# Kernel optimization log

Hardware: AMD Instinct MI355X
Metric: run time of the kernel (lower is better)

The kernel has to match this reference:

```python
import jax, jax.numpy as jnp
import numpy as np

B, S, D_IN, H, D_K = 4, 2048, 512, 8, 64
EPS = 1e-5

def _layer_norm(x, gamma, beta):
    mu = jnp.mean(x, axis=-1, keepdims=True)
    var = jnp.var(x, axis=-1, keepdims=True)
    return (x - mu) * jax.lax.rsqrt(var + EPS) * gamma + beta

def setup_inputs() -> dict:
    key = jax.random.key(0)
    ks = jax.random.split(key, 8)
    d_model = H * D_K
    scale = 1.0 / np.sqrt(D_IN)
    inp = {
        "q": jax.random.normal(ks[0], (B, S, D_IN), jnp.float32),
        "k": jax.random.normal(ks[1], (B, S, D_IN), jnp.float32),
        "v": jax.random.normal(ks[2], (B, S, D_IN), jnp.float32),
        "mask": jnp.ones((B, 1, S, S), jnp.float32),
        "Wq": jax.random.normal(ks[3], (D_IN, d_model), jnp.float32) * scale,
        "bq": jnp.zeros((d_model,), jnp.float32),
        "Wk": jax.random.normal(ks[4], (D_IN, d_model), jnp.float32) * scale,
        "bk": jnp.zeros((d_model,), jnp.float32),
        "Wv": jax.random.normal(ks[5], (D_IN, d_model), jnp.float32) * scale,
        "bv": jnp.zeros((d_model,), jnp.float32),
        "Wo": jax.random.normal(ks[6], (d_model, D_IN), jnp.float32) * (1.0 / np.sqrt(d_model)),
        "bo": jnp.zeros((D_IN,), jnp.float32),
        "gamma": jnp.ones((D_IN,), jnp.float32),
        "beta": jnp.zeros((D_IN,), jnp.float32),
    }
    return inp

def reference(q, k, v, mask, Wq, bq, Wk, bk, Wv, bv, Wo, bo, gamma, beta):
    b, sq, _ = q.shape
    # QKV projections, split heads: [B,S,H*Dk] -> [B,H,S,Dk]
    qh = (q @ Wq + bq).reshape(b, sq, H, D_K).transpose(0, 2, 1, 3)
    kh = (k @ Wk + bk).reshape(b, -1, H, D_K).transpose(0, 2, 1, 3)
    vh = (v @ Wv + bv).reshape(b, -1, H, D_K).transpose(0, 2, 1, 3)
    # scores with multiplicative mask + threshold (non-standard, per source)
    scores = jnp.einsum('bhqd,bhkd->bhqk', qh, kh) / np.sqrt(D_K)
    scores = scores * mask  # mask broadcasts over heads (repeat in torch)
    scores = jnp.where(scores > 0, scores, jnp.float32(-10000.0))
    attn = jax.nn.softmax(scores, axis=-1)
    out = jnp.einsum('bhqk,bhkd->bhqd', attn, vh)
    out = out.transpose(0, 2, 1, 3).reshape(b, sq, H * D_K)
    out = out @ Wo + bo
    return _layer_norm(q + out, gamma, beta)
```

## Files before the change

kernel.cpp:

```cpp
#include <hip/hip_runtime.h>
#include <stdint.h>

typedef __attribute__((ext_vector_type(8))) short s16x8;
typedef __attribute__((ext_vector_type(4))) float f32x4;

__device__ __forceinline__ unsigned short f2bf(float f){
  union { float f; unsigned u; } v; v.f = f;
  return (unsigned short)((v.u + 0x7FFFu + ((v.u>>16)&1u))>>16);
}
__device__ __forceinline__ float bf2f(unsigned short u){
  union { unsigned u; float f; } c; c.u = ((unsigned)u)<<16; return c.f;
}
#if __has_builtin(__builtin_amdgcn_cvt_pk_bf16_f32)
__device__ __forceinline__ unsigned pkbf(float a, float b){
  typedef __attribute__((ext_vector_type(2))) __bf16 bf16x2;
  union { bf16x2 v; unsigned u; } c;
  c.v = __builtin_amdgcn_cvt_pk_bf16_f32(a, b);
  return c.u;
}
#else
__device__ __forceinline__ unsigned pkbf(float a, float b){
  return (unsigned)f2bf(a) | ((unsigned)f2bf(b)<<16);
}
#endif

__device__ __forceinline__ void g2l16(const void* g, void* l){
  auto* lp = reinterpret_cast<__attribute__((address_space(3))) unsigned int*>(
      reinterpret_cast<uintptr_t>(l));
  auto* gp = reinterpret_cast<const __attribute__((address_space(1))) unsigned int*>(
      reinterpret_cast<uintptr_t>(g));
  __builtin_amdgcn_global_load_lds(gp, lp, 16, 0, 0);
}

__global__ __launch_bounds__(256) void cvt_all(
    const float* __restrict__ mask, const float* __restrict__ q,
    const float* __restrict__ k,    const float* __restrict__ v,
    unsigned short* __restrict__ mo, unsigned short* __restrict__ qo,
    unsigned short* __restrict__ ko, unsigned short* __restrict__ vo)
{
  const int z = blockIdx.z;
  const float* src = (z==0)?mask:(z==1)?q:(z==2)?k:v;
  unsigned short* dst = (z==0)?mo:(z==1)?qo:(z==2)?ko:vo;
  const int n = (z==0) ? 4*2048*2048 : 8192*512;
  const int i8 = (blockIdx.x*256 + threadIdx.x)*8;
  if (i8 < n){
    const float4 a = *(const float4*)&src[i8];
    const float4 b = *(const float4*)&src[i8+4];
    uint4 o;
    o.x = pkbf(a.x,a.y); o.y = pkbf(a.z,a.w);
    o.z = pkbf(b.x,b.y); o.w = pkbf(b.z,b.w);
    *(uint4*)&dst[i8] = o;
  }
}

__global__ __launch_bounds__(256) void convert_wT(
    const float* __restrict__ W0, const float* __restrict__ W1,
    const float* __restrict__ W2, const float* __restrict__ W3,
    unsigned short* __restrict__ T0, unsigned short* __restrict__ T1,
    unsigned short* __restrict__ T2, unsigned short* __restrict__ T3)
{
  __shared__ float Ts[64][65];
  const int z = blockIdx.z;
  const float* W = (z==0)?W0:(z==1)?W1:(z==2)?W2:W3;
  unsigned short* Wt = (z==0)?T0:(z==1)?T1:(z==2)?T2:T3;
  const int t = threadIdx.x;
  const int k0 = blockIdx.x*64, n0 = blockIdx.y*64;
  {
    const int r = t>>4, c = (t&15)*4;
#pragma unroll
    for (int rr=0; rr<4; ++rr){
      const float4 w4 = *(const float4*)&W[(size_t)(k0 + r + rr*16)*512 + n0 + c];
      Ts[r+rr*16][c]   = w4.x; Ts[r+rr*16][c+1] = w4.y;
      Ts[r+rr*16][c+2] = w4.z; Ts[r+rr*16][c+3] = w4.w;
    }
  }
  __syncthreads();
  const int n = t>>2, kc = (t&3)*16;
  unsigned o[8];
#pragma unroll
  for (int i=0;i<16;i+=2) o[i>>1] = pkbf(Ts[kc+i][n], Ts[kc+i+1][n]);
  *(uint4*)&Wt[(size_t)(n0+n)*512 + k0 + kc]     = *(uint4*)&o[0];
  *(uint4*)&Wt[(size_t)(n0+n)*512 + k0 + kc + 8] = *(uint4*)&o[4];
}

template<int EPI>
__global__ __launch_bounds__(256) void gemm_m97(
    const unsigned short* __restrict__ A0, const unsigned short* __restrict__ A1,
    const unsigned short* __restrict__ A2,
    const unsigned short* __restrict__ W0, const unsigned short* __restrict__ W1,
    const unsigned short* __restrict__ W2,
    const float* __restrict__ b0, const float* __restrict__ b1, const float* __restrict__ b2,
    unsigned short* __restrict__ Oq, unsigned short* __restrict__ Ok,
    unsigned short* __restrict__ Ov, unsigned short* __restrict__ Oflat)
{
  __shared__ unsigned short As[128*64];
  __shared__ unsigned short Bs[128*64];
  const int t = threadIdx.x;
  const int lane = t & 63;
  const int w = t >> 6;
  const int l16 = lane & 15;
  const int quad = lane >> 4;
  const int wm = w & 1, wn = w >> 1;
  const int bm = blockIdx.x, bn = blockIdx.y;
  const int z = (EPI==0) ? (int)blockIdx.z : 0;
  const unsigned short* A  = (z==0)?A0:(z==1)?A1:A2;
  const unsigned short* Wt = (z==0)?W0:(z==1)?W1:W2;
  const float* bias        = (z==0)?b0:(z==1)?b1:b2;

  const int Lr = lane >> 3;
  const int gc = (lane & 7) ^ Lr;

  f32x4 acc[4][4];
#pragma unroll
  for(int i=0;i<4;i++)
#pragma unroll
    for(int j=0;j<4;j++) acc[i][j] = (f32x4){0.f,0.f,0.f,0.f};

  for (int kt=0; kt<8; ++kt){
    const int k0 = kt*64;
#pragma unroll
    for (int j=0;j<4;++j){
      const int rb = w*32 + j*8;
      g2l16(&A [(size_t)(bm*128 + rb + Lr)*512 + k0 + gc*8], &As[rb*64]);
      g2l16(&Wt[(size_t)(bn*128 + rb + Lr)*512 + k0 + gc*8], &Bs[rb*64]);
    }
    __syncthreads();
#pragma unroll
    for (int kk=0;kk<2;++kk){
      s16x8 af[4], bfr[4];
#pragma unroll
      for (int mt=0;mt<4;++mt){
        const int row = wm*64 + mt*16 + l16;
        af[mt] = *(const s16x8*)&As[row*64 + (((kk*4+quad) ^ (row&7))*8)];
      }
#pragma unroll
      for (int nt=0;nt<4;++nt){
        const int row = wn*64 + nt*16 + l16;
        bfr[nt] = *(const s16x8*)&Bs[row*64 + (((kk*4+quad) ^ (row&7))*8)];
      }
#pragma unroll
      for (int mt=0;mt<4;++mt)
#pragma unroll
        for (int nt=0;nt<4;++nt)
          acc[mt][nt] = __builtin_amdgcn_mfma_f32_16x16x32_bf16(af[mt], bfr[nt], acc[mt][nt], 0,0,0);
    }
    __syncthreads();
  }

#pragma unroll
  for (int mt=0;mt<4;++mt){
    const int gm = bm*128 + wm*64 + mt*16 + quad*4;
    const int b_ = gm>>11, s = gm & 2047;
#pragma unroll
    for (int nt=0;nt<4;++nt){
      const int gn = bn*128 + wn*64 + nt*16 + l16;
      const float bv = bias[gn];
      if (EPI==1){
#pragma unroll
        for (int r=0;r<4;++r)
          Oflat[(size_t)(gm+r)*512 + gn] = f2bf(acc[mt][nt][r] + bv);
      } else if (z==2){
        const int hh = gn>>6, dk = gn&63;
        uint2 uu;
        uu.x = pkbf(acc[mt][nt][0]+bv, acc[mt][nt][1]+bv);
        uu.y = pkbf(acc[mt][nt][2]+bv, acc[mt][nt][3]+bv);
        *(uint2*)&Ov[(((size_t)b_*8 + hh)*64 + dk)*2048 + s] = uu;
      } else {
        const int hh = gn>>6, dk = gn&63;
        unsigned short* Out = (z==0)?Oq:Ok;
        const float scl = (z==0)?0.125f:1.0f;
#pragma unroll
        for (int r=0;r<4;++r)
          Out[(((size_t)b_*8 + hh)*2048 + (s+r))*64 + dk] = f2bf((acc[mt][nt][r]+bv)*scl);
      }
    }
  }
}

__global__ __launch_bounds__(512,4) void attn_kernel(
    const unsigned short* __restrict__ Qp, const unsigned short* __restrict__ Kp,
    const unsigned short* __restrict__ Vt, const unsigned short* __restrict__ maskb,
    unsigned short* __restrict__ Ap)
{
  __shared__ unsigned short Ks[2][64*64];
  __shared__ unsigned short Vs[2][64*64];
  const int t = threadIdx.x;
  const int lane = t & 63;
  const int w = t >> 6;
  const int l16 = lane & 15;
  const int quad = lane >> 4;
  const int h = blockIdx.x, qt = blockIdx.y, b = blockIdx.z;
  const int q0 = qt*128;
  const unsigned short* Qb = Qp + (((size_t)b*8 + h)*2048 + q0)*64;
  const unsigned short* Kb = Kp + ((size_t)b*8 + h)*2048*64;
  const unsigned short* Vb = Vt + ((size_t)b*8 + h)*64*2048;
  const unsigned short* mb = maskb + (size_t)b*2048*2048;

  s16x8 qf[2];
#pragma unroll
  for (int kk=0;kk<2;++kk)
    qf[kk] = *(const s16x8*)&Qb[(size_t)(w*16 + l16)*64 + kk*32 + quad*8];

  const int Lr = lane >> 3;
  const int gc = (lane & 7) ^ Lr;
  const int srow = w*8 + Lr;

  g2l16(&Kb[(size_t)srow*64   + gc*8], &Ks[0][w*8*64]);
  g2l16(&Vb[(size_t)srow*2048 + gc*8], &Vs[0][w*8*64]);

  f32x4 o_acc[4];
#pragma unroll
  for(int nt=0;nt<4;++nt) o_acc[nt]=(f32x4){0.f,0.f,0.f,0.f};
  float l_run = 0.f;

  union U8 { unsigned u[4]; s16x8 v; };
  const int gq = q0 + w*16 + l16;

  for (int kt=0; kt<32; ++kt){
    const int cur = kt&1;
    const int kbase = kt*64;
    __syncthreads();

    uint2 mr[4];
    {
      const unsigned short* mrow = mb + (size_t)gq*2048 + kbase + quad*4;
#pragma unroll
      for (int nt=0;nt<4;++nt) mr[nt] = *(const uint2*)&mrow[nt*16];
    }
    if (kt<31){
      const int kb2 = (kt+1)*64;
      g2l16(&Kb[(size_t)(kb2+srow)*64 + gc*8],   &Ks[cur^1][w*8*64]);
      g2l16(&Vb[(size_t)srow*2048 + kb2 + gc*8], &Vs[cur^1][w*8*64]);
    }

    f32x4 sc[4];
#pragma unroll
    for(int nt=0;nt<4;++nt) sc[nt]=(f32x4){0.f,0.f,0.f,0.f};
#pragma unroll
    for (int nt=0;nt<4;++nt){
      const int row = nt*16 + l16;
      const int rx = row & 7;
      const s16x8 kf0 = *(const s16x8*)&Ks[cur][row*64 + ((quad ^ rx)*8)];
      const s16x8 kf1 = *(const s16x8*)&Ks[cur][row*64 + (((4+quad) ^ rx)*8)];
      sc[nt] = __builtin_amdgcn_mfma_f32_16x16x32_bf16(kf0, qf[0], sc[nt],0,0,0);
      sc[nt] = __builtin_amdgcn_mfma_f32_16x16x32_bf16(kf1, qf[1], sc[nt],0,0,0);
    }
    unsigned pk[8];
    float rs = 0.f;
#pragma unroll
    for (int nt=0;nt<4;++nt){
      const float m0 = bf2f((unsigned short)(mr[nt].x & 0xffffu));
      const float m1 = bf2f((unsigned short)(mr[nt].x >> 16));
      const float m2 = bf2f((unsigned short)(mr[nt].y & 0xffffu));
      const float m3 = bf2f((unsigned short)(mr[nt].y >> 16));
      float x0 = sc[nt][0]*m0, x1 = sc[nt][1]*m1, x2 = sc[nt][2]*m2, x3 = sc[nt][3]*m3;
      x0 = (x0>0.f)?x0:-10000.f; x1 = (x1>0.f)?x1:-10000.f;
      x2 = (x2>0.f)?x2:-10000.f; x3 = (x3>0.f)?x3:-10000.f;
      const float e0 = __expf(x0), e1 = __expf(x1), e2 = __expf(x2), e3 = __expf(x3);
      rs += (e0+e1)+(e2+e3);
      pk[nt*2]   = pkbf(e0, e1);
      pk[nt*2+1] = pkbf(e2, e3);
    }
    rs += __shfl_xor(rs, 16);
    rs += __shfl_xor(rs, 32);
    l_run += rs;
    U8 pu[2];
#pragma unroll
    for (int kk=0;kk<2;++kk)
#pragma unroll
      for (int c=0;c<4;++c){
        const int srcLane = (((quad&1)*2 + (c>>1))<<4) | l16;
        const int vA = __shfl((int)pk[kk*4 + (c&1)],     srcLane);
        const int vB = __shfl((int)pk[kk*4 + 2 + (c&1)], srcLane);
        pu[kk].u[c] = (quad < 2) ? (unsigned)vA : (unsigned)vB;
      }
#pragma unroll
    for (int nt=0;nt<4;++nt){
      const int row = nt*16 + l16;
      const int rx = row & 7;
      const s16x8 vf0 = *(const s16x8*)&Vs[cur][row*64 + ((quad ^ rx)*8)];
      const s16x8 vf1 = *(const s16x8*)&Vs[cur][row*64 + (((4+quad) ^ rx)*8)];
      o_acc[nt] = __builtin_amdgcn_mfma_f32_16x16x32_bf16(vf0, pu[0].v, o_acc[nt],0,0,0);
      o_acc[nt] = __builtin_amdgcn_mfma_f32_16x16x32_bf16(vf1, pu[1].v, o_acc[nt],0,0,0);
    }
  }
  {
    const float inv = 1.0f / l_run;
#pragma unroll
    for (int nt=0;nt<4;++nt){
      uint2 uu;
      uu.x = pkbf(o_acc[nt][0]*inv, o_acc[nt][1]*inv);
      uu.y = pkbf(o_acc[nt][2]*inv, o_acc[nt][3]*inv);
      *(uint2*)&Ap[((size_t)b*2048 + gq)*512 + h*64 + nt*16 + quad*4] = uu;
    }
  }
}

__global__ __launch_bounds__(256) void ln_kernel(
    const float* __restrict__ q, const unsigned short* __restrict__ O2,
    const float* __restrict__ gamma, const float* __restrict__ beta,
    float* __restrict__ out)
{
  const int r = blockIdx.x;
  const int t = threadIdx.x;
  const float* xq = q + (size_t)r * 512;
  const unsigned short* xo = O2 + (size_t)r * 512;
  const float x0 = xq[t]       + bf2f(xo[t]);
  const float x1 = xq[t + 256] + bf2f(xo[t + 256]);
  float s  = x0 + x1;
  float ss = x0*x0 + x1*x1;
#pragma unroll
  for (int off = 1; off < 64; off <<= 1) {
    s  += __shfl_xor(s, off);
    ss += __shfl_xor(ss, off);
  }
  __shared__ float ssum[4], ssq[4];
  const int w = t >> 6;
  if ((t & 63) == 0) { ssum[w] = s; ssq[w] = ss; }
  __syncthreads();
  const float S4 = ssum[0] + ssum[1] + ssum[2] + ssum[3];
  const float Q4 = ssq[0] + ssq[1] + ssq[2] + ssq[3];
  const float mu   = S4 * (1.0f / 512.0f);
  const float var  = Q4 * (1.0f / 512.0f) - mu * mu;
  const float rstd = rsqrtf(var + 1e-5f);
  out[(size_t)r*512 + t]       = (x0 - mu)*rstd*gamma[t] + beta[t];
  out[(size_t)r*512 + t + 256] = (x1 - mu)*rstd*gamma[t+256] + beta[t+256];
}

extern "C" void kernel_launch(void* const* d_in, const int* in_sizes, int n_in,
                              void* d_out, int out_size, void* d_ws, size_t ws_size,
                              hipStream_t stream)
{
  (void)in_sizes; (void)n_in; (void)out_size; (void)ws_size;
  const float* q    = (const float*)d_in[0];
  const float* k    = (const float*)d_in[1];
  const float* v    = (const float*)d_in[2];
  const float* mask = (const float*)d_in[3];
  const float* Wq   = (const float*)d_in[4];
  const float* bq   = (const float*)d_in[5];
  const float* Wk   = (const float*)d_in[6];
  const float* bk   = (const float*)d_in[7];
  const float* Wv   = (const float*)d_in[8];
  const float* bv   = (const float*)d_in[9];
  const float* Wo   = (const float*)d_in[10];
  const float* bo   = (const float*)d_in[11];
  const float* gamma = (const float*)d_in[12];
  const float* beta  = (const float*)d_in[13];
  float* out = (float*)d_out;

  const size_t NT = (size_t)8192*512;
  unsigned short* WtQ  = (unsigned short*)d_ws;
  unsigned short* WtK  = WtQ + 512*512;
  unsigned short* WtV  = WtK + 512*512;
  unsigned short* WtO  = WtV + 512*512;
  unsigned short* Mb   = WtO + 512*512;
  unsigned short* qb   = Mb + (size_t)4*2048*2048;
  unsigned short* kb   = qb + NT;
  unsigned short* vb   = kb + NT;
  unsigned short* Qp   = vb + NT;
  unsigned short* Kp   = Qp + NT;
  unsigned short* Vtg  = Kp + NT;
  unsigned short* Ap   = Vtg + NT;
  unsigned short* O2b  = Ap + NT;

  cvt_all<<<dim3(8192,1,4), 256, 0, stream>>>(mask, q, k, v, Mb, qb, kb, vb);
  convert_wT<<<dim3(8,8,4), 256, 0, stream>>>(Wq, Wk, Wv, Wo, WtQ, WtK, WtV, WtO);
  gemm_m97<0><<<dim3(64,4,3), 256, 0, stream>>>(qb, kb, vb, WtQ, WtK, WtV,
                                                bq, bk, bv, Qp, Kp, Vtg, nullptr);
  attn_kernel<<<dim3(8,16,4), 512, 0, stream>>>(Qp, Kp, Vtg, Mb, Ap);
  gemm_m97<1><<<dim3(64,4,1), 256, 0, stream>>>(Ap, nullptr, nullptr, WtO, nullptr, nullptr,
                                                bo, nullptr, nullptr,
                                                nullptr, nullptr, nullptr, O2b);
  ln_kernel<<<dim3(8192), 256, 0, stream>>>(q, O2b, gamma, beta, out);
}
```

Before: 311.3 us.

## Read fp32 mask directly in attention and give each wave two query tiles

Removes the separate fp32-to-bf16 pass over the full mask and its bf16 workspace copy, so the attention kernel now reads the fp32 mask itself. The attention block drops from 8 waves to 4, and each wave handles 32 query rows (two 16-row tiles), so every K/V fragment read from LDS feeds two MFMAs. K and V LDS tiles get a new fragment-ordered, padded layout. The trade-off is twice as many mask bytes read inside the attention loop per step, higher register pressure from the doubled accumulators, and fewer waves per block.

```diff
diff --git a/kernel.cpp b/kernel.cpp
--- a/kernel.cpp
+++ b/kernel.cpp
@@ -32,25 +32,20 @@
   __builtin_amdgcn_global_load_lds(gp, lp, 16, 0, 0);
 }
 
-__global__ __launch_bounds__(256) void cvt_all(
-    const float* __restrict__ mask, const float* __restrict__ q,
-    const float* __restrict__ k,    const float* __restrict__ v,
-    unsigned short* __restrict__ mo, unsigned short* __restrict__ qo,
-    unsigned short* __restrict__ ko, unsigned short* __restrict__ vo)
+__global__ __launch_bounds__(256) void cvt_qkv(
+    const float* __restrict__ q, const float* __restrict__ k, const float* __restrict__ v,
+    unsigned short* __restrict__ qo, unsigned short* __restrict__ ko, unsigned short* __restrict__ vo)
 {
   const int z = blockIdx.z;
-  const float* src = (z==0)?mask:(z==1)?q:(z==2)?k:v;
-  unsigned short* dst = (z==0)?mo:(z==1)?qo:(z==2)?ko:vo;
-  const int n = (z==0) ? 4*2048*2048 : 8192*512;
+  const float* src = (z==0)?q:(z==1)?k:v;
+  unsigned short* dst = (z==0)?qo:(z==1)?ko:vo;
   const int i8 = (blockIdx.x*256 + threadIdx.x)*8;
-  if (i8 < n){
-    const float4 a = *(const float4*)&src[i8];
-    const float4 b = *(const float4*)&src[i8+4];
-    uint4 o;
-    o.x = pkbf(a.x,a.y); o.y = pkbf(a.z,a.w);
-    o.z = pkbf(b.x,b.y); o.w = pkbf(b.z,b.w);
-    *(uint4*)&dst[i8] = o;
-  }
+  const float4 a = *(const float4*)&src[i8];
+  const float4 b = *(const float4*)&src[i8+4];
+  uint4 o;
+  o.x = pkbf(a.x,a.y); o.y = pkbf(a.z,a.w);
+  o.z = pkbf(b.x,b.y); o.w = pkbf(b.z,b.w);
+  *(uint4*)&dst[i8] = o;
 }
 
 __global__ __launch_bounds__(256) void convert_wT(
@@ -177,121 +172,141 @@
   }
 }
 
-__global__ __launch_bounds__(512,4) void attn_kernel(
+__global__ __launch_bounds__(256,2) void attn_kernel(
     const unsigned short* __restrict__ Qp, const unsigned short* __restrict__ Kp,
-    const unsigned short* __restrict__ Vt, const unsigned short* __restrict__ maskb,
+    const unsigned short* __restrict__ Vt, const float* __restrict__ mask,
     unsigned short* __restrict__ Ap)
 {
-  __shared__ unsigned short Ks[2][64*64];
-  __shared__ unsigned short Vs[2][64*64];
+  __shared__ unsigned short Ks[2][8*512];
+  __shared__ unsigned short Vs[2][8*528];
   const int t = threadIdx.x;
   const int lane = t & 63;
   const int w = t >> 6;
   const int l16 = lane & 15;
   const int quad = lane >> 4;
   const int h = blockIdx.x, qt = blockIdx.y, b = blockIdx.z;
-  const int q0 = qt*128;
-  const unsigned short* Qb = Qp + (((size_t)b*8 + h)*2048 + q0)*64;
+  const int q0 = qt*128 + w*32;
+  const unsigned short* Qb = Qp + ((size_t)b*8 + h)*2048*64;
   const unsigned short* Kb = Kp + ((size_t)b*8 + h)*2048*64;
   const unsigned short* Vb = Vt + ((size_t)b*8 + h)*64*2048;
-  const unsigned short* mb = maskb + (size_t)b*2048*2048;
-
-  s16x8 qf[2];
-#pragma unroll
-  for (int kk=0;kk<2;++kk)
-    qf[kk] = *(const s16x8*)&Qb[(size_t)(w*16 + l16)*64 + kk*32 + quad*8];
-
-  const int Lr = lane >> 3;
-  const int gc = (lane & 7) ^ Lr;
-  const int srow = w*8 + Lr;
-
-  g2l16(&Kb[(size_t)srow*64   + gc*8], &Ks[0][w*8*64]);
-  g2l16(&Vb[(size_t)srow*2048 + gc*8], &Vs[0][w*8*64]);
-
-  f32x4 o_acc[4];
-#pragma unroll
-  for(int nt=0;nt<4;++nt) o_acc[nt]=(f32x4){0.f,0.f,0.f,0.f};
-  float l_run = 0.f;
+  const float* mb = mask + (size_t)b*2048*2048;
+
+  s16x8 qf[2][2];
+#pragma unroll
+  for (int tc=0;tc<2;++tc)
+#pragma unroll
+    for (int kk=0;kk<2;++kk)
+      qf[tc][kk] = *(const s16x8*)&Qb[(size_t)(q0 + tc*16 + l16)*64 + kk*32 + quad*8];
+
+  int koffs[2], voffs[2];
+#pragma unroll
+  for (int j=0;j<2;++j){
+    koffs[j] = ((w*16 + (lane&15))*64) + ((j*4 + (lane>>4))*8);
+    voffs[j] = (((2*w+j)*8 + (lane>>3))*2048) + (((lane&7) ^ (lane>>3))*8);
+  }
+#pragma unroll
+  for (int j=0;j<2;++j){
+    g2l16(Kb + koffs[j], &Ks[0][(2*w+j)*512]);
+    g2l16(Vb + voffs[j], &Vs[0][(2*w+j)*528]);
+  }
+
+  f32x4 o_acc[2][4];
+#pragma unroll
+  for(int tc=0;tc<2;++tc)
+#pragma unroll
+    for(int nt=0;nt<4;++nt) o_acc[tc][nt]=(f32x4){0.f,0.f,0.f,0.f};
+  float l_run[2] = {0.f, 0.f};
+
+  const int b3 = l16>>3, a7 = l16&7;
+  const float* mrow0 = mb + (size_t)(q0 + l16)*2048 + quad*4;
+  const float* mrow1 = mrow0 + (size_t)16*2048;
 
   union U8 { unsigned u[4]; s16x8 v; };
-  const int gq = q0 + w*16 + l16;
 
   for (int kt=0; kt<32; ++kt){
     const int cur = kt&1;
     const int kbase = kt*64;
     __syncthreads();
 
-    uint2 mr[4];
-    {
-      const unsigned short* mrow = mb + (size_t)gq*2048 + kbase + quad*4;
-#pragma unroll
-      for (int nt=0;nt<4;++nt) mr[nt] = *(const uint2*)&mrow[nt*16];
+    float4 mr[2][4];
+#pragma unroll
+    for (int nt=0;nt<4;++nt){
+      mr[0][nt] = *(const float4*)&mrow0[kbase + nt*16];
+      mr[1][nt] = *(const float4*)&mrow1[kbase + nt*16];
     }
     if (kt<31){
       const int kb2 = (kt+1)*64;
-      g2l16(&Kb[(size_t)(kb2+srow)*64 + gc*8],   &Ks[cur^1][w*8*64]);
-      g2l16(&Vb[(size_t)srow*2048 + kb2 + gc*8], &Vs[cur^1][w*8*64]);
-    }
-
-    f32x4 sc[4];
-#pragma unroll
-    for(int nt=0;nt<4;++nt) sc[nt]=(f32x4){0.f,0.f,0.f,0.f};
-#pragma unroll
-    for (int nt=0;nt<4;++nt){
-      const int row = nt*16 + l16;
-      const int rx = row & 7;
-      const s16x8 kf0 = *(const s16x8*)&Ks[cur][row*64 + ((quad ^ rx)*8)];
-      const s16x8 kf1 = *(const s16x8*)&Ks[cur][row*64 + (((4+quad) ^ rx)*8)];
-      sc[nt] = __builtin_amdgcn_mfma_f32_16x16x32_bf16(kf0, qf[0], sc[nt],0,0,0);
-      sc[nt] = __builtin_amdgcn_mfma_f32_16x16x32_bf16(kf1, qf[1], sc[nt],0,0,0);
-    }
-    unsigned pk[8];
-    float rs = 0.f;
-#pragma unroll
-    for (int nt=0;nt<4;++nt){
-      const float m0 = bf2f((unsigned short)(mr[nt].x & 0xffffu));
-      const float m1 = bf2f((unsigned short)(mr[nt].x >> 16));
-      const float m2 = bf2f((unsigned short)(mr[nt].y & 0xffffu));
-      const float m3 = bf2f((unsigned short)(mr[nt].y >> 16));
-      float x0 = sc[nt][0]*m0, x1 = sc[nt][1]*m1, x2 = sc[nt][2]*m2, x3 = sc[nt][3]*m3;
-      x0 = (x0>0.f)?x0:-10000.f; x1 = (x1>0.f)?x1:-10000.f;
-      x2 = (x2>0.f)?x2:-10000.f; x3 = (x3>0.f)?x3:-10000.f;
-      const float e0 = __expf(x0), e1 = __expf(x1), e2 = __expf(x2), e3 = __expf(x3);
-      rs += (e0+e1)+(e2+e3);
-      pk[nt*2]   = pkbf(e0, e1);
-      pk[nt*2+1] = pkbf(e2, e3);
-    }
-    rs += __shfl_xor(rs, 16);
-    rs += __shfl_xor(rs, 32);
-    l_run += rs;
-    U8 pu[2];
-#pragma unroll
-    for (int kk=0;kk<2;++kk)
-#pragma unroll
-      for (int c=0;c<4;++c){
-        const int srcLane = (((quad&1)*2 + (c>>1))<<4) | l16;
-        const int vA = __shfl((int)pk[kk*4 + (c&1)],     srcLane);
-        const int vB = __shfl((int)pk[kk*4 + 2 + (c&1)], srcLane);
-        pu[kk].u[c] = (quad < 2) ? (unsigned)vA : (unsigned)vB;
-      }
-#pragma unroll
-    for (int nt=0;nt<4;++nt){
-      const int row = nt*16 + l16;
-      const int rx = row & 7;
-      const s16x8 vf0 = *(const s16x8*)&Vs[cur][row*64 + ((quad ^ rx)*8)];
-      const s16x8 vf1 = *(const s16x8*)&Vs[cur][row*64 + (((4+quad) ^ rx)*8)];
-      o_acc[nt] = __builtin_amdgcn_mfma_f32_16x16x32_bf16(vf0, pu[0].v, o_acc[nt],0,0,0);
-      o_acc[nt] = __builtin_amdgcn_mfma_f32_16x16x32_bf16(vf1, pu[1].v, o_acc[nt],0,0,0);
-    }
-  }
-  {
-    const float inv = 1.0f / l_run;
-#pragma unroll
-    for (int nt=0;nt<4;++nt){
+#pragma unroll
+      for (int j=0;j<2;++j){
+        g2l16(Kb + (size_t)kb2*64 + koffs[j], &Ks[cur^1][(2*w+j)*512]);
+        g2l16(Vb + kb2 + voffs[j],            &Vs[cur^1][(2*w+j)*528]);
+      }
+    }
+
+    f32x4 sc[2][4];
+#pragma unroll
+    for(int tc=0;tc<2;++tc)
+#pragma unroll
+      for(int nt=0;nt<4;++nt) sc[tc][nt]=(f32x4){0.f,0.f,0.f,0.f};
+#pragma unroll
+    for (int nt=0;nt<4;++nt)
+#pragma unroll
+      for (int kk=0;kk<2;++kk){
+        const s16x8 kf = *(const s16x8*)&Ks[cur][(nt*2+kk)*512 + lane*8];
+#pragma unroll
+        for (int tc=0;tc<2;++tc)
+          sc[tc][nt] = __builtin_amdgcn_mfma_f32_16x16x32_bf16(kf, qf[tc][kk], sc[tc][nt],0,0,0);
+      }
+
+#pragma unroll
+    for (int tc=0;tc<2;++tc){
+      unsigned pk[8];
+      float rs = 0.f;
+#pragma unroll
+      for (int nt=0;nt<4;++nt){
+        float x0 = sc[tc][nt][0]*mr[tc][nt].x, x1 = sc[tc][nt][1]*mr[tc][nt].y;
+        float x2 = sc[tc][nt][2]*mr[tc][nt].z, x3 = sc[tc][nt][3]*mr[tc][nt].w;
+        x0 = (x0>0.f)?x0:-10000.f; x1 = (x1>0.f)?x1:-10000.f;
+        x2 = (x2>0.f)?x2:-10000.f; x3 = (x3>0.f)?x3:-10000.f;
+        const float e0 = __expf(x0), e1 = __expf(x1), e2 = __expf(x2), e3 = __expf(x3);
+        rs += (e0+e1)+(e2+e3);
+        pk[nt*2]   = pkbf(e0, e1);
+        pk[nt*2+1] = pkbf(e2, e3);
+      }
+      rs += __shfl_xor(rs, 16);
+      rs += __shfl_xor(rs, 32);
+      l_run[tc] += rs;
+      U8 pu[2];
+#pragma unroll
+      for (int kk=0;kk<2;++kk)
+#pragma unroll
+        for (int c=0;c<4;++c){
+          const int srcLane = (((quad&1)*2 + (c>>1))<<4) | l16;
+          const int vA = __shfl((int)pk[kk*4 + (c&1)],     srcLane);
+          const int vB = __shfl((int)pk[kk*4 + 2 + (c&1)], srcLane);
+          pu[kk].u[c] = (quad < 2) ? (unsigned)vA : (unsigned)vB;
+        }
+#pragma unroll
+      for (int ot=0;ot<4;++ot){
+#pragma unroll
+        for (int kk=0;kk<2;++kk){
+          const s16x8 vf = *(const s16x8*)&Vs[cur][(ot*2+b3)*528 + a7*64 + (((kk*4+quad)^a7)*8)];
+          o_acc[tc][ot] = __builtin_amdgcn_mfma_f32_16x16x32_bf16(vf, pu[kk].v, o_acc[tc][ot],0,0,0);
+        }
+      }
+    }
+  }
+
+#pragma unroll
+  for (int tc=0;tc<2;++tc){
+    const float inv = 1.0f / l_run[tc];
+    const int gq = q0 + tc*16 + l16;
+#pragma unroll
+    for (int ot=0;ot<4;++ot){
       uint2 uu;
-      uu.x = pkbf(o_acc[nt][0]*inv, o_acc[nt][1]*inv);
-      uu.y = pkbf(o_acc[nt][2]*inv, o_acc[nt][3]*inv);
-      *(uint2*)&Ap[((size_t)b*2048 + gq)*512 + h*64 + nt*16 + quad*4] = uu;
+      uu.x = pkbf(o_acc[tc][ot][0]*inv, o_acc[tc][ot][1]*inv);
+      uu.y = pkbf(o_acc[tc][ot][2]*inv, o_acc[tc][ot][3]*inv);
+      *(uint2*)&Ap[((size_t)b*2048 + gq)*512 + h*64 + ot*16 + quad*4] = uu;
     }
   }
 }
@@ -353,8 +368,7 @@
   unsigned short* WtK  = WtQ + 512*512;
   unsigned short* WtV  = WtK + 512*512;
   unsigned short* WtO  = WtV + 512*512;
-  unsigned short* Mb   = WtO + 512*512;
-  unsigned short* qb   = Mb + (size_t)4*2048*2048;
+  unsigned short* qb   = WtO + 512*512;
   unsigned short* kb   = qb + NT;
   unsigned short* vb   = kb + NT;
   unsigned short* Qp   = vb + NT;
@@ -363,11 +377,11 @@
   unsigned short* Ap   = Vtg + NT;
   unsigned short* O2b  = Ap + NT;
 
-  cvt_all<<<dim3(8192,1,4), 256, 0, stream>>>(mask, q, k, v, Mb, qb, kb, vb);
+  cvt_qkv<<<dim3(2048,1,3), 256, 0, stream>>>(q, k, v, qb, kb, vb);
   convert_wT<<<dim3(8,8,4), 256, 0, stream>>>(Wq, Wk, Wv, Wo, WtQ, WtK, WtV, WtO);
   gemm_m97<0><<<dim3(64,4,3), 256, 0, stream>>>(qb, kb, vb, WtQ, WtK, WtV,
                                                 bq, bk, bv, Qp, Kp, Vtg, nullptr);
-  attn_kernel<<<dim3(8,16,4), 512, 0, stream>>>(Qp, Kp, Vtg, Mb, Ap);
+  attn_kernel<<<dim3(8,16,4), 256, 0, stream>>>(Qp, Kp, Vtg, mask, Ap);
   gemm_m97<1><<<dim3(64,4,1), 256, 0, stream>>>(Ap, nullptr, nullptr, WtO, nullptr, nullptr,
                                                 bo, nullptr, nullptr,
                                                 nullptr, nullptr, nullptr, O2b);
```

New measurement: 349.1 us. 12.2% more time.
